# Optimization experiments

Measured on AMD Instinct MI355X. Metric: run time of the kernel, lower is better.

Reference implementation:

```python
import jax, jax.numpy as jnp
import numpy as np
import math

# ---- static ERP sampling-grid construction (matches ERPGridGenerator) ----
def make_grid(H, W, Kh=3, Kw=3, Sh=2, Sw=2, alpha=0.8, eps=1e-3, max_scale=4.0):
    H_out = (H + Sh - 1) // Sh
    W_out = (W + Sw - 1) // Sw
    off_h = np.arange(-(Kh // 2), Kh // 2 + 1)
    off_w = np.arange(-(Kw // 2), Kw // 2 + 1).astype(np.float32)
    phi = ((np.arange(H).astype(np.float32) + 0.5) / H) * math.pi - math.pi / 2.0
    cos_all = np.clip(np.abs(np.cos(phi)), eps, None)
    ih_center = np.minimum(np.arange(H_out) * Sh, H - 1)
    rows = np.clip(ih_center[:, None] + off_h[None, :], 0, H - 1)          # [H_out,Kh]
    d_w = np.clip(alpha / cos_all[rows], None, max_scale).astype(np.float32)  # [H_out,Kh]
    jw = ((np.arange(W_out) * Sw) % W).astype(np.float32)                  # [W_out]
    # lon/lat index tensors [H_out,W_out,Kh,Kw]
    lon = np.round(jw[None, :, None, None] + d_w[:, None, :, None] * off_w[None, None, None, :]) % W
    lat = np.broadcast_to(rows[:, None, :, None].astype(np.float32), lon.shape)
    y = 2.0 * (lat + 0.5) / H - 1.0
    x = 2.0 * (lon + 0.5) / W - 1.0
    grid = np.stack([x, y], axis=-1).reshape(H_out * Kh, W_out * Kw, 2)    # same C-order reshape as torch
    return jnp.asarray(grid.astype(np.float32))

# ---- bilinear grid_sample, padding_mode='border', align_corners=False ----
def grid_sample_border(x, grid):
    # x: [B,C,H,W], grid: [Hg,Wg,2] in [-1,1] -> out [B,C,Hg,Wg]
    H, W = x.shape[2], x.shape[3]
    ix = jnp.clip((grid[..., 0] + 1.0) * 0.5 * W - 0.5, 0.0, W - 1.0)
    iy = jnp.clip((grid[..., 1] + 1.0) * 0.5 * H - 0.5, 0.0, H - 1.0)
    x0 = jnp.floor(ix); y0 = jnp.floor(iy)
    wx = ix - x0; wy = iy - y0
    x0i = x0.astype(jnp.int32); y0i = y0.astype(jnp.int32)
    x1i = jnp.minimum(x0i + 1, W - 1); y1i = jnp.minimum(y0i + 1, H - 1)
    v00 = x[:, :, y0i, x0i]; v01 = x[:, :, y0i, x1i]
    v10 = x[:, :, y1i, x0i]; v11 = x[:, :, y1i, x1i]
    top = v00 * (1.0 - wx) + v01 * wx
    bot = v10 * (1.0 - wx) + v11 * wx
    return top * (1.0 - wy) + bot * wy

def conv2d(x, w, stride=1):
    return jax.lax.conv_general_dilated(x, w, (stride, stride), 'VALID',
                                        dimension_numbers=('NCHW', 'OIHW', 'NCHW'))

def avg_pool3(x):
    s = jax.lax.reduce_window(x, 0.0, jax.lax.add, (1, 1, 3, 3), (1, 1, 3, 3), 'VALID')
    return s / 9.0

def sphere_conv(x, w):
    H, W = x.shape[2], x.shape[3]
    grid = make_grid(H, W)
    xu = grid_sample_border(x, grid)      # [B,C,3*H_out,3*W_out]
    return avg_pool3(conv2d(xu, w, 1))    # [B,Cout,H_out-1,W_out-1]

def bn(x, g, b, m, v, eps=1e-5):
    inv = g / jnp.sqrt(v + eps)
    return x * inv[None, :, None, None] + (b - m * inv)[None, :, None, None]

def lrelu(x):
    return jnp.where(x >= 0, x, 0.05 * x)

def gru_cell(x, h, wih, whh, bih, bhh):
    gi = x @ wih.T + bih
    gh = h @ whh.T + bhh
    i_r, i_z, i_n = jnp.split(gi, 3, axis=-1)
    h_r, h_z, h_n = jnp.split(gh, 3, axis=-1)
    r = jax.nn.sigmoid(i_r + h_r)
    z = jax.nn.sigmoid(i_z + h_z)
    n = jnp.tanh(i_n + r * h_n)
    return (1.0 - z) * n + z * h


def setup_inputs() -> dict:
    key = jax.random.key(0)
    ks = jax.random.split(key, 48)
    B = 256
    def rn(k, shape, s=1.0):
        return jax.random.normal(k, shape, dtype=jnp.float32) * s
    inp = {}
    inp['x'] = rn(ks[0], (B, 6, 64, 128))
    inp['v'] = rn(ks[1], (B, 9))
    inp['hx'] = rn(ks[2], (B, 256), 0.1)
    def add_bn(i, c, pre):
        inp[pre + '_g'] = 1.0 + rn(ks[i], (c,), 0.1)
        inp[pre + '_b'] = rn(ks[i + 1], (c,), 0.1)
        inp[pre + '_m'] = rn(ks[i + 2], (c,), 0.1)
        inp[pre + '_v'] = jax.random.uniform(ks[i + 3], (c,), dtype=jnp.float32) * 0.5 + 0.5
    inp['sc0_w'] = rn(ks[3], (32, 6, 3, 3), 0.1);   add_bn(4, 32, 'bn0')
    inp['sc1_w'] = rn(ks[8], (64, 32, 3, 3), 0.06); add_bn(9, 64, 'bn1')
    inp['c2_w'] = rn(ks[13], (64, 64, 3, 3), 0.04); add_bn(14, 64, 'bn2')
    inp['c3_w'] = rn(ks[18], (64, 64, 2, 2), 0.06); add_bn(19, 64, 'bn3')
    inp['c4_w'] = rn(ks[23], (128, 64, 3, 3), 0.04); add_bn(24, 128, 'bn4')
    inp['c5_w'] = rn(ks[28], (128, 128, 3, 3), 0.03); add_bn(29, 128, 'bn5')
    inp['proj_w'] = rn(ks[33], (256, 2560), 0.02)
    inp['vproj_w'] = rn(ks[34], (256, 9), 0.2)
    inp['vproj_b'] = rn(ks[35], (256,), 0.1)
    inp['gru_wih'] = rn(ks[36], (768, 256), 0.05)
    inp['gru_whh'] = rn(ks[37], (768, 256), 0.05)
    inp['gru_bih'] = rn(ks[38], (768,), 0.05)
    inp['gru_bhh'] = rn(ks[39], (768,), 0.05)
    inp['fc_w'] = rn(ks[40], (4, 256), 0.01)
    return inp


def reference(x, v, hx,
              sc0_w, bn0_g, bn0_b, bn0_m, bn0_v,
              sc1_w, bn1_g, bn1_b, bn1_m, bn1_v,
              c2_w, bn2_g, bn2_b, bn2_m, bn2_v,
              c3_w, bn3_g, bn3_b, bn3_m, bn3_v,
              c4_w, bn4_g, bn4_b, bn4_m, bn4_v,
              c5_w, bn5_g, bn5_b, bn5_m, bn5_v,
              proj_w, vproj_w, vproj_b,
              gru_wih, gru_whh, gru_bih, gru_bhh, fc_w):
    # stem0: SphereConv2d -> BN -> LeakyReLU, twice
    h = lrelu(bn(sphere_conv(x, sc0_w), bn0_g, bn0_b, bn0_m, bn0_v))   # [B,32,31,63]
    h = lrelu(bn(sphere_conv(h, sc1_w), bn1_g, bn1_b, bn1_m, bn1_v))   # [B,64,15,31]
    # stem1: plain convs
    h = lrelu(bn(conv2d(h, c2_w, 1), bn2_g, bn2_b, bn2_m, bn2_v))      # [B,64,13,29]
    h = lrelu(bn(conv2d(h, c3_w, 2), bn3_g, bn3_b, bn3_m, bn3_v))      # [B,64,6,14]
    h = lrelu(bn(conv2d(h, c4_w, 1), bn4_g, bn4_b, bn4_m, bn4_v))      # [B,128,4,12]
    h = lrelu(bn(conv2d(h, c5_w, 1), bn5_g, bn5_b, bn5_m, bn5_v))      # [B,128,2,10]
    img_feat = h.reshape(h.shape[0], -1) @ proj_w.T                     # [B,256]
    fused = lrelu(img_feat + v @ vproj_w.T + vproj_b)
    hx_new = gru_cell(fused, hx, gru_wih, gru_whh, gru_bih, gru_bhh)
    act = lrelu(hx_new) @ fc_w.T                                        # [B,4]
    return (act, hx_new)
```

## Files before the change

kernel.cpp:

```cpp
#include <hip/hip_runtime.h>
#include <math.h>

typedef unsigned short u16;
typedef unsigned int   u32;
typedef __attribute__((ext_vector_type(8))) _Float16 half8;
typedef __attribute__((ext_vector_type(4))) float    f32x4;

#define PI_F 3.14159265358979323846f

__device__ __forceinline__ float lrelu_f(float x){ return x >= 0.f ? x : 0.05f*x; }
__device__ __forceinline__ u16 f2h(float f){ _Float16 h = (_Float16)f; u16 u; __builtin_memcpy(&u,&h,2); return u; }
__device__ __forceinline__ float h2f(u16 u){ _Float16 h; __builtin_memcpy(&h,&u,2); return (float)h; }

struct PrepP {
    int *map0; u16 *map1h;
    const float *sc0_w, *sc1_w;
    u16 *wb0, *wb1;
    const float *c2_w, *c3_w, *c4_w, *c5_w;
    u16 *wb2, *wb3, *wb4, *wb5;
    const float *pw, *wih, *whh;
    u16 *pwh, *wihh, *whhh;
};

template<typename T>
__device__ void d_map(T* map, int H, int W, int Wo, int total, int i)
{
    if (i >= total) return;
    int oh  = i / (Wo*9);
    int rem = i % (Wo*9);
    int ow  = rem / 9;
    int r2  = rem % 9;
    int kh  = r2/3, kw = r2%3;
    int ihc = min(oh*2, H-1);
    int lat = min(max(ihc + kh - 1, 0), H-1);
    float phi = ((float)lat + 0.5f)/(float)H * PI_F - 0.5f*PI_F;
    float ca  = fmaxf(fabsf(cosf(phi)), 1e-3f);
    float d   = fminf(0.8f/ca, 4.0f);
    float jw  = (float)((ow*2) % W);
    float lonf = rintf(jw + d*(float)(kw-1));
    int lon = (int)lonf % W; if (lon < 0) lon += W;
    map[i] = (T)(lat*W + lon);
}

__device__ void d_wsph(const float* w3, u16* wh, int CO, int CI, int CIP,
                       int TPC, int NCH, int KCd, int KCm, int total, int i)
{
    if (i >= total) return;
    int j = i % KCm, t = i / KCm;
    int ch = t % NCH, co = t / NCH;
    float s = 0.f;
    if (j < KCd){
        int tl = j / CIP, ci = j % CIP;
        int tap = ch*TPC + tl;
        if (ci < CI && tap < 25){
            int u = tap/5, v = tap%5;
            const float* w = w3 + (co*CI + ci)*9;
            int pl0 = max(0, u-2), pl1 = min(2, u);
            int q0 = max(0, v-2), q1 = min(2, v);
            for (int pl=pl0; pl<=pl1; ++pl)
                for (int q=q0; q<=q1; ++q) s += w[pl*3+q];
            s *= (1.0f/9.0f);
        }
    }
    wh[i] = f2h(s);
}

__device__ void d_wdir(const float* w, u16* wh, int CO, int CI, int TPC,
                       int NCH, int KPQ, int KCm, int total, int i)
{
    if (i >= total) return;
    int j = i % KCm, t = i / KCm;
    int ch = t % NCH, co = t / NCH;
    int tl = j / CI, ci = j % CI;
    int tap = ch*TPC + tl;
    wh[i] = f2h(w[(size_t)(co*CI + ci)*KPQ + tap]);
}

__global__ void k_prep(PrepP p)
{
    int i = blockIdx.x*blockDim.x + threadIdx.x;
    switch (blockIdx.y){
    case 0:  d_map<int>(p.map0, 64, 128, 64, 18432, i); break;
    case 1:  d_map<u16>(p.map1h, 31, 63, 32, 4608, i); break;
    case 2:  d_wsph(p.sc0_w, p.wb0, 32,  6,  8, 13, 2, 104, 128,  8192, i); break;
    case 3:  d_wsph(p.sc1_w, p.wb1, 64, 32, 32,  5, 5, 160, 160, 51200, i); break;
    case 4:  d_wdir(p.c2_w, p.wb2,  64,  64, 3, 3, 9, 192,  36864, i); break;
    case 5:  d_wdir(p.c3_w, p.wb3,  64,  64, 2, 2, 4, 128,  16384, i); break;
    case 6:  d_wdir(p.c4_w, p.wb4, 128,  64, 3, 3, 9, 192,  73728, i); break;
    case 7:  d_wdir(p.c5_w, p.wb5, 128, 128, 1, 9, 9, 128, 147456, i); break;
    case 8:  if (i < 256*2560){
                 int n = i / 2560, k = i % 2560;
                 int pos = k >> 7, co = k & 127;
                 p.pwh[i] = f2h(p.pw[(size_t)n*2560 + co*20 + pos]);
             } break;
    case 9:  if (i < 768*256) p.wihh[i] = f2h(p.wih[i]); break;
    default: if (i < 768*256) p.whhh[i] = f2h(p.whh[i]); break;
    }
}

__global__ void k_xu0(const float* __restrict__ x, const int* __restrict__ map,
                      u16* __restrict__ out)
{
    int p = blockIdx.x*blockDim.x + threadIdx.x;
    int b = blockIdx.y;
    int m = map[p];
    const float* xb = x + (size_t)b*6*8192 + m;
    u16 v[8];
    #pragma unroll
    for (int c=0;c<6;++c) v[c] = f2h(xb[c*8192]);
    v[6]=0; v[7]=0;
    *reinterpret_cast<uint4*>(out + ((size_t)b*18432 + p)*8) =
        *reinterpret_cast<uint4*>(v);
}

template<int BT,int CO,int OW,int NTOT,int NB,int IH,int IW,int KW,int S,int CI,
         int TPC,int NCH,int KCm,int KCp,int WR,int WC,int WN,int WM,
         int GATHER=0,int INTOT=0,int MAPSZ=1>
__global__ __launch_bounds__(BT) void k_nconv(
    const u16* __restrict__ in, const u16* __restrict__ map,
    const u16* __restrict__ wh,
    const float* __restrict__ bg, const float* __restrict__ bb,
    const float* __restrict__ bm, const float* __restrict__ bv,
    u16* __restrict__ out)
{
    constexpr int NT_N = WR*WN;
    constexpr int NPAD = NT_N*16;
    constexpr int KCd  = TPC*CI;
    constexpr int CIV  = CI/8;
    static_assert(WR*WC == BT/64, "waves cover block");
    static_assert(WC*WM*16 == CO, "co tiling covers CO");
    static_assert(CI % 8 == 0, "16B staging vectors");
    static_assert(KCm % 32 == 0 && KCp % 8 == 0 && KCd <= KCm, "tiling");
    static_assert((NPAD & (NPAD-1)) == 0, "NPAD pow2");
    static_assert(!GATHER || MAPSZ >= IH*IW, "LDS map covers raster");
    __shared__ __align__(16) u16 sA[NPAD*KCp];
    __shared__ __align__(16) u16 sB[CO*KCp];
    __shared__ u16 smap[GATHER ? MAPSZ : 2];

    int b  = blockIdx.x / NB;
    int n0 = (blockIdx.x % NB)*NPAD;
    int tid = threadIdx.x;
    const u16* xb = in + (GATHER ? (size_t)b*INTOT*CI : (size_t)b*IH*IW*CI);

    if constexpr (GATHER){
        for (int i = tid; i < MAPSZ; i += BT) smap[i] = map[i];
    }
    if constexpr (KCm > KCd){
        constexpr int PADW = KCm - KCd;
        for (int e = tid; e < NPAD*PADW; e += BT)
            sA[(e/PADW)*KCp + KCd + e%PADW] = 0;
    }
    if constexpr (GATHER) __syncthreads();

    int w = tid >> 6, lane = tid & 63, l15 = lane & 15, l4 = lane >> 4;
    int wr = w / WC, wc = w % WC;
    f32x4 acc[WN][WM];
    #pragma unroll
    for (int i=0;i<WN;++i)
        #pragma unroll
        for (int j=0;j<WM;++j) acc[i][j] = (f32x4){0.f,0.f,0.f,0.f};

    for (int ch = 0; ch < NCH; ++ch){
        if (ch) __syncthreads();
        constexpr int ITER = NPAD*TPC*CIV;
        for (int i = tid; i < ITER; i += BT){
            int n_l = i / (TPC*CIV);
            int r   = i - n_l*(TPC*CIV);
            int tl  = r / CIV;
            int civ = r - tl*CIV;
            int n_g = min(n0 + n_l, NTOT-1);
            int oh = n_g/OW, ow = n_g - oh*OW;
            int tap = ch*TPC + tl;
            int u = tap/KW, v = tap - u*KW;
            int pos = (oh*S + u)*IW + ow*S + v;
            const u16* src;
            if constexpr (GATHER){
                int m = (int)smap[pos];
                src = xb + (size_t)m*CI + civ*8;
            } else {
                src = xb + (size_t)pos*CI + civ*8;
            }
            uint4 val = *reinterpret_cast<const uint4*>(src);
            *reinterpret_cast<uint4*>(&sA[n_l*KCp + tl*CI + civ*8]) = val;
        }
        constexpr int W8 = KCm/8;
        for (int i = tid; i < CO*W8; i += BT){
            int co = i / W8, j = (i - co*W8)*8;
            uint4 v = *reinterpret_cast<const uint4*>(wh + ((size_t)co*NCH + ch)*KCm + j);
            *reinterpret_cast<uint4*>(&sB[co*KCp + j]) = v;
        }
        __syncthreads();
        #pragma unroll
        for (int ks = 0; ks < KCm/32; ++ks){
            half8 a[WN], bf[WM];
            #pragma unroll
            for (int i=0;i<WN;++i)
                a[i] = *reinterpret_cast<const half8*>(
                    &sA[((wr*WN+i)*16 + l15)*KCp + ks*32 + l4*8]);
            #pragma unroll
            for (int j=0;j<WM;++j)
                bf[j] = *reinterpret_cast<const half8*>(
                    &sB[((wc*WM+j)*16 + l15)*KCp + ks*32 + l4*8]);
            #pragma unroll
            for (int i=0;i<WN;++i)
                #pragma unroll
                for (int j=0;j<WM;++j)
                    acc[i][j] = __builtin_amdgcn_mfma_f32_16x16x32_f16(a[i], bf[j], acc[i][j], 0, 0, 0);
        }
    }
    #pragma unroll
    for (int j=0;j<WM;++j){
        int co = (wc*WM+j)*16 + l15;
        float inv = bg[co]*rsqrtf(bv[co]+1e-5f);
        float shv = bb[co] - bm[co]*inv;
        #pragma unroll
        for (int i=0;i<WN;++i){
            #pragma unroll
            for (int r=0;r<4;++r){
                int gn = n0 + (wr*WN+i)*16 + l4*4 + r;
                if (gn < NTOT)
                    out[((size_t)b*NTOT + gn)*CO + co] = f2h(lrelu_f(fmaf(acc[i][j][r], inv, shv)));
            }
        }
    }
}

__global__ __launch_bounds__(256) void k_head2(
    const u16* __restrict__ h5, const u16* __restrict__ pwh,
    const float* __restrict__ vin, const float* __restrict__ vproj_w,
    const float* __restrict__ vproj_b, u16* __restrict__ fusedh)
{
    __shared__ __align__(16) u16 sA[64*136];
    __shared__ __align__(16) u16 sB[64*136];
    __shared__ float sv[64*9];
    int m0 = blockIdx.x*64, nc0 = blockIdx.y*64;
    int tid = threadIdx.x;
    int w = tid >> 6, lane = tid & 63, l15 = lane & 15, l4 = lane >> 4;
    f32x4 acc[4];
    #pragma unroll
    for (int j=0;j<4;++j) acc[j] = (f32x4){0.f,0.f,0.f,0.f};

    for (int i = tid; i < 576; i += 256) sv[i] = vin[(m0 + i/9)*9 + i%9];

    for (int kc0 = 0; kc0 < 2560; kc0 += 128){
        if (kc0) __syncthreads();
        for (int i = tid; i < 1024; i += 256){
            int r = i >> 4, jv = (i & 15)*8;
            *reinterpret_cast<uint4*>(&sA[r*136 + jv]) =
                *reinterpret_cast<const uint4*>(h5 + (size_t)(m0+r)*2560 + kc0 + jv);
            *reinterpret_cast<uint4*>(&sB[r*136 + jv]) =
                *reinterpret_cast<const uint4*>(pwh + (size_t)(nc0+r)*2560 + kc0 + jv);
        }
        __syncthreads();
        #pragma unroll
        for (int ks = 0; ks < 4; ++ks){
            half8 a = *reinterpret_cast<const half8*>(&sA[(w*16 + l15)*136 + ks*32 + l4*8]);
            #pragma unroll
            for (int j=0;j<4;++j){
                half8 bf = *reinterpret_cast<const half8*>(&sB[(j*16 + l15)*136 + ks*32 + l4*8]);
                acc[j] = __builtin_amdgcn_mfma_f32_16x16x32_f16(a, bf, acc[j], 0, 0, 0);
            }
        }
    }
    #pragma unroll
    for (int j=0;j<4;++j){
        int nc = nc0 + j*16 + l15;
        float bias = vproj_b[nc];
        #pragma unroll
        for (int r=0;r<4;++r){
            int ml = w*16 + l4*4 + r;
            float av = 0.f;
            #pragma unroll
            for (int k=0;k<9;++k) av = fmaf(sv[ml*9+k], vproj_w[nc*9+k], av);
            fusedh[(size_t)(m0+ml)*256 + nc] = f2h(lrelu_f(acc[j][r] + av + bias));
        }
    }
}

__global__ __launch_bounds__(256) void k_ggemm(
    const u16* __restrict__ fusedh, const float* __restrict__ hx,
    const u16* __restrict__ wihh, const u16* __restrict__ whhh,
    float* __restrict__ gbuf)
{
    __shared__ __align__(16) u16 sA[64*136];
    __shared__ __align__(16) u16 sB[64*136];
    int m0 = blockIdx.x*64;
    int t  = blockIdx.y;
    int half = t / 12, nt = t - half*12;
    int n0 = nt*64;
    const u16* B = (half ? whhh : wihh) + (size_t)n0*256;
    int tid = threadIdx.x;
    int w = tid >> 6, lane = tid & 63, l15 = lane & 15, l4 = lane >> 4;
    f32x4 acc[4];
    #pragma unroll
    for (int j=0;j<4;++j) acc[j] = (f32x4){0.f,0.f,0.f,0.f};

    for (int kc0 = 0; kc0 < 256; kc0 += 128){
        if (kc0) __syncthreads();
        for (int i = tid; i < 1024; i += 256){
            int r = i >> 4, jv = (i & 15)*8;
            if (half == 0){
                *reinterpret_cast<uint4*>(&sA[r*136 + jv]) =
                    *reinterpret_cast<const uint4*>(fusedh + (size_t)(m0+r)*256 + kc0 + jv);
            } else {
                const float* src = hx + (size_t)(m0+r)*256 + kc0 + jv;
                float4 f0 = *reinterpret_cast<const float4*>(src);
                float4 f1 = *reinterpret_cast<const float4*>(src+4);
                u16 v[8] = { f2h(f0.x),f2h(f0.y),f2h(f0.z),f2h(f0.w),
                             f2h(f1.x),f2h(f1.y),f2h(f1.z),f2h(f1.w) };
                *reinterpret_cast<uint4*>(&sA[r*136 + jv]) = *reinterpret_cast<uint4*>(v);
            }
            *reinterpret_cast<uint4*>(&sB[r*136 + jv]) =
                *reinterpret_cast<const uint4*>(B + (size_t)r*256 + kc0 + jv);
        }
        __syncthreads();
        #pragma unroll
        for (int ks = 0; ks < 4; ++ks){
            half8 a = *reinterpret_cast<const half8*>(&sA[(w*16 + l15)*136 + ks*32 + l4*8]);
            #pragma unroll
            for (int j=0;j<4;++j){
                half8 bf = *reinterpret_cast<const half8*>(&sB[(j*16 + l15)*136 + ks*32 + l4*8]);
                acc[j] = __builtin_amdgcn_mfma_f32_16x16x32_f16(a, bf, acc[j], 0, 0, 0);
            }
        }
    }
    #pragma unroll
    for (int j=0;j<4;++j){
        int nc = half*768 + n0 + j*16 + l15;
        #pragma unroll
        for (int r=0;r<4;++r){
            int m = m0 + w*16 + l4*4 + r;
            gbuf[(size_t)m*1536 + nc] = acc[j][r];
        }
    }
}

__global__ __launch_bounds__(256) void k_gate_act(
    const float* __restrict__ gbuf, const float* __restrict__ hx,
    const float* __restrict__ bih, const float* __restrict__ bhh,
    const float* __restrict__ fc_w,
    float* __restrict__ hx_new, float* __restrict__ act)
{
    __shared__ float sh[256];
    int b = blockIdx.x, j = threadIdx.x;
    const float* g = gbuf + (size_t)b*1536;
    float ir = g[j]       + bih[j];
    float iz = g[256+j]   + bih[256+j];
    float in_= g[512+j]   + bih[512+j];
    float hr = g[768+j]   + bhh[j];
    float hz = g[1024+j]  + bhh[256+j];
    float hn = g[1280+j]  + bhh[512+j];
    float r = 1.f/(1.f+expf(-(ir+hr)));
    float z = 1.f/(1.f+expf(-(iz+hz)));
    float n = tanhf(in_ + r*hn);
    float h = (1.f-z)*n + z*hx[b*256+j];
    hx_new[b*256+j] = h;
    sh[j] = lrelu_f(h);
    __syncthreads();
    int w = j >> 6, lane = j & 63;
    const float* fw = fc_w + w*256;
    int k0 = lane*4;
    float a = sh[k0]*fw[k0] + sh[k0+1]*fw[k0+1] + sh[k0+2]*fw[k0+2] + sh[k0+3]*fw[k0+3];
    #pragma unroll
    for (int off = 32; off; off >>= 1) a += __shfl_down(a, off);
    if (lane == 0) act[b*4 + w] = a;
}

extern "C" void kernel_launch(void* const* d_in, const int* in_sizes, int n_in,
                              void* d_out, int out_size, void* d_ws, size_t ws_size,
                              hipStream_t stream)
{
    const float* x      = (const float*)d_in[0];
    const float* vin    = (const float*)d_in[1];
    const float* hx     = (const float*)d_in[2];
    const float* sc0_w  = (const float*)d_in[3];
    const float* bn0g   = (const float*)d_in[4];
    const float* bn0b   = (const float*)d_in[5];
    const float* bn0m   = (const float*)d_in[6];
    const float* bn0v   = (const float*)d_in[7];
    const float* sc1_w  = (const float*)d_in[8];
    const float* bn1g   = (const float*)d_in[9];
    const float* bn1b   = (const float*)d_in[10];
    const float* bn1m   = (const float*)d_in[11];
    const float* bn1v   = (const float*)d_in[12];
    const float* c2_w   = (const float*)d_in[13];
    const float* bn2g   = (const float*)d_in[14];
    const float* bn2b   = (const float*)d_in[15];
    const float* bn2m   = (const float*)d_in[16];
    const float* bn2v   = (const float*)d_in[17];
    const float* c3_w   = (const float*)d_in[18];
    const float* bn3g   = (const float*)d_in[19];
    const float* bn3b   = (const float*)d_in[20];
    const float* bn3m   = (const float*)d_in[21];
    const float* bn3v   = (const float*)d_in[22];
    const float* c4_w   = (const float*)d_in[23];
    const float* bn4g   = (const float*)d_in[24];
    const float* bn4b   = (const float*)d_in[25];
    const float* bn4m   = (const float*)d_in[26];
    const float* bn4v   = (const float*)d_in[27];
    const float* c5_w   = (const float*)d_in[28];
    const float* bn5g   = (const float*)d_in[29];
    const float* bn5b   = (const float*)d_in[30];
    const float* bn5m   = (const float*)d_in[31];
    const float* bn5v   = (const float*)d_in[32];
    const float* proj_w = (const float*)d_in[33];
    const float* vproj_w= (const float*)d_in[34];
    const float* vproj_b= (const float*)d_in[35];
    const float* gru_wih= (const float*)d_in[36];
    const float* gru_whh= (const float*)d_in[37];
    const float* gru_bih= (const float*)d_in[38];
    const float* gru_bhh= (const float*)d_in[39];
    const float* fc_w   = (const float*)d_in[40];

    char* base = (char*)d_ws;
    size_t off = 0;
    auto alloc = [&](size_t bytes)->char*{
        char* p = base + off; off += (bytes + 255) & ~(size_t)255; return p;
    };
    int* map0 = (int*)alloc((size_t)96*192*4);
    u16* map1h= (u16*)alloc((size_t)48*96*2);
    u16* wb0  = (u16*)alloc((size_t)32*2*128*2);
    u16* wb1  = (u16*)alloc((size_t)64*5*160*2);
    u16* wb2  = (u16*)alloc((size_t)64*3*192*2);
    u16* wb3  = (u16*)alloc((size_t)64*2*128*2);
    u16* wb4  = (u16*)alloc((size_t)128*3*192*2);
    u16* wb5  = (u16*)alloc((size_t)128*9*128*2);
    u16* pwh  = (u16*)alloc((size_t)256*2560*2);
    u16* wihh = (u16*)alloc((size_t)768*256*2);
    u16* whhh = (u16*)alloc((size_t)768*256*2);
    u16* xu   = (u16*)alloc((size_t)256*18432*8*2);
    u16* h0   = (u16*)alloc((size_t)256*1953*32*2);
    u16* h1   = (u16*)alloc((size_t)256*465*64*2);
    u16* h2   = (u16*)alloc((size_t)256*377*64*2);
    u16* h3   = (u16*)alloc((size_t)256*84*64*2);
    u16* h4   = (u16*)alloc((size_t)256*48*128*2);
    u16* h5   = (u16*)alloc((size_t)256*20*128*2);
    u16* fusedh = (u16*)alloc((size_t)256*256*2);
    float* gbuf = (float*)alloc((size_t)256*1536*4);

    PrepP pp = { map0, map1h, sc0_w, sc1_w, wb0, wb1,
                 c2_w, c3_w, c4_w, c5_w, wb2, wb3, wb4, wb5,
                 proj_w, gru_wih, gru_whh, pwh, wihh, whhh };
    k_prep<<<dim3(2560, 11), 256, 0, stream>>>(pp);

    k_xu0<<<dim3(72, 256), 256, 0, stream>>>(x, map0, xu);
    k_nconv<512,32,63,1953,8, 96,192, 5,3, 8,13,2, 128,136, 8,1,2,2>
        <<<256*8, 512, 0, stream>>>(xu, nullptr, wb0, bn0g,bn0b,bn0m,bn0v, h0);
    k_nconv<512,64,31,465,4, 48,96, 5,3, 32,5,5, 160,168, 4,2,2,2, 1,1953,4608>
        <<<256*4, 512, 0, stream>>>(h0, map1h, wb1, bn1g,bn1b,bn1m,bn1v, h1);
    k_nconv<512,64,29,377,3, 15,31, 3,1, 64,3,3, 192,200, 4,2,2,2>
        <<<256*3, 512, 0, stream>>>(h1, nullptr, wb2, bn2g,bn2b,bn2m,bn2v, h2);
    k_nconv<256,64,14,84,3, 13,29, 2,2, 64,2,2, 128,136, 2,2,1,2>
        <<<256*3, 256, 0, stream>>>(h2, nullptr, wb3, bn3g,bn3b,bn3m,bn3v, h3);
    k_nconv<256,128,12,48,3, 6,14, 3,1, 64,3,3, 192,200, 1,4,1,2>
        <<<256*3, 256, 0, stream>>>(h3, nullptr, wb4, bn4g,bn4b,bn4m,bn4v, h4);
    k_nconv<256,128,10,20,2, 4,12, 3,1, 128,1,9, 128,136, 1,4,1,2>
        <<<256*2, 256, 0, stream>>>(h4, nullptr, wb5, bn5g,bn5b,bn5m,bn5v, h5);

    k_head2<<<dim3(4,4), 256, 0, stream>>>(h5, pwh, vin, vproj_w, vproj_b, fusedh);
    k_ggemm<<<dim3(4,24), 256, 0, stream>>>(fusedh, hx, wihh, whhh, gbuf);
    float* outp = (float*)d_out;
    k_gate_act<<<256, 256, 0, stream>>>(gbuf, hx, gru_bih, gru_bhh, fc_w,
                                        outp + 1024, outp);
}
```

Baseline: 258.6 us.

## Prefetch next activation chunk into registers during MFMA compute in conv kernel

New measurement: 377.9 us. +46.1%, slower.

```diff
diff --git a/kernel.cpp b/kernel.cpp
--- a/kernel.cpp
+++ b/kernel.cpp
@@ -127,6 +127,8 @@
     constexpr int NPAD = NT_N*16;
     constexpr int KCd  = TPC*CI;
     constexpr int CIV  = CI/8;
+    constexpr int ITER = NPAD*TPC*CIV;
+    constexpr int RPT  = (ITER + BT - 1)/BT;
     static_assert(WR*WC == BT/64, "waves cover block");
     static_assert(WC*WM*16 == CO, "co tiling covers CO");
     static_assert(CI % 8 == 0, "16B staging vectors");
@@ -160,35 +162,58 @@
         #pragma unroll
         for (int j=0;j<WM;++j) acc[i][j] = (f32x4){0.f,0.f,0.f,0.f};
 
+    uint4 rbuf[RPT];
+
+    auto load_chunk = [&](int ch){
+        #pragma unroll
+        for (int r=0;r<RPT;++r){
+            int i = tid + r*BT;
+            if (ITER % BT == 0 || i < ITER){
+                int n_l = i / (TPC*CIV);
+                int rr  = i - n_l*(TPC*CIV);
+                int tl  = rr / CIV;
+                int civ = rr - tl*CIV;
+                int n_g = min(n0 + n_l, NTOT-1);
+                int oh = n_g/OW, ow = n_g - oh*OW;
+                int tap = ch*TPC + tl;
+                int u = tap/KW, v = tap - u*KW;
+                int pos = (oh*S + u)*IW + ow*S + v;
+                const u16* src;
+                if constexpr (GATHER){
+                    int m = (int)smap[pos];
+                    src = xb + (size_t)m*CI + civ*8;
+                } else {
+                    src = xb + (size_t)pos*CI + civ*8;
+                }
+                rbuf[r] = *reinterpret_cast<const uint4*>(src);
+            }
+        }
+    };
+    auto write_chunk = [&](){
+        #pragma unroll
+        for (int r=0;r<RPT;++r){
+            int i = tid + r*BT;
+            if (ITER % BT == 0 || i < ITER){
+                int n_l = i / (TPC*CIV);
+                int rr  = i - n_l*(TPC*CIV);
+                int tl  = rr / CIV;
+                int civ = rr - tl*CIV;
+                *reinterpret_cast<uint4*>(&sA[n_l*KCp + tl*CI + civ*8]) = rbuf[r];
+            }
+        }
+    };
+
+    load_chunk(0);
     for (int ch = 0; ch < NCH; ++ch){
         if (ch) __syncthreads();
-        constexpr int ITER = NPAD*TPC*CIV;
-        for (int i = tid; i < ITER; i += BT){
-            int n_l = i / (TPC*CIV);
-            int r   = i - n_l*(TPC*CIV);
-            int tl  = r / CIV;
-            int civ = r - tl*CIV;
-            int n_g = min(n0 + n_l, NTOT-1);
-            int oh = n_g/OW, ow = n_g - oh*OW;
-            int tap = ch*TPC + tl;
-            int u = tap/KW, v = tap - u*KW;
-            int pos = (oh*S + u)*IW + ow*S + v;
-            const u16* src;
-            if constexpr (GATHER){
-                int m = (int)smap[pos];
-                src = xb + (size_t)m*CI + civ*8;
-            } else {
-                src = xb + (size_t)pos*CI + civ*8;
-            }
-            uint4 val = *reinterpret_cast<const uint4*>(src);
-            *reinterpret_cast<uint4*>(&sA[n_l*KCp + tl*CI + civ*8]) = val;
-        }
+        write_chunk();
         constexpr int W8 = KCm/8;
         for (int i = tid; i < CO*W8; i += BT){
             int co = i / W8, j = (i - co*W8)*8;
             uint4 v = *reinterpret_cast<const uint4*>(wh + ((size_t)co*NCH + ch)*KCm + j);
             *reinterpret_cast<uint4*>(&sB[co*KCp + j]) = v;
         }
+        if (ch + 1 < NCH) load_chunk(ch + 1);
         __syncthreads();
         #pragma unroll
         for (int ks = 0; ks < KCm/32; ++ks){
```
